# Kernel tuning notes

Hardware: AMD Instinct MI355X
Metric: run time of the kernel (lower is better)

The kernel has to match this reference:

```python
import jax, jax.numpy as jnp
import numpy as np

B, N, C = 128, 36, 1024
K_NB = 16            # neighbors per node (top-k, includes loop)
KERNEL = 8           # number of Gaussian kernels
OUT = 1024           # out_dim; per-kernel out = OUT // KERNEL
PI = np.float32(np.pi)


def setup_inputs() -> dict:
    key = jax.random.key(0)
    ks = jax.random.split(key, 9)
    node_feats = jax.random.normal(ks[0], (B, N, C), dtype=jnp.float32)
    node_centre = jax.random.uniform(ks[1], (B, N, 2), dtype=jnp.float32)
    neighbor_idx = jax.random.randint(ks[2], (B * N, K_NB), 0, B * N, dtype=jnp.int32)
    graph_weights = jax.random.uniform(ks[3], (B * N * K_NB, 1), dtype=jnp.float32)
    # Gaussian kernel params (per reset_parameters)
    mean_rho = jax.random.uniform(ks[4], (1, KERNEL), dtype=jnp.float32)
    mean_theta = jax.random.uniform(ks[5], (1, KERNEL), minval=-PI, maxval=PI, dtype=jnp.float32)
    precision_rho = jax.random.uniform(ks[6], (1, KERNEL), minval=0.5, maxval=1.0, dtype=jnp.float32)
    precision_theta = jax.random.uniform(ks[7], (1, KERNEL), minval=0.5, maxval=1.0, dtype=jnp.float32)
    # per-kernel Linear(node_dim, out_dim//kernel, bias=False), stacked: [K, d_out_k, C]
    conv_w = jax.random.normal(ks[8], (KERNEL, OUT // KERNEL, C), dtype=jnp.float32) * (1.0 / np.sqrt(C))
    return {
        "node_feats": node_feats,
        "node_centre": node_centre,
        "neighbor_idx": neighbor_idx,
        "graph_weights": graph_weights,
        "mean_rho": mean_rho,
        "mean_theta": mean_theta,
        "precision_rho": precision_rho,
        "precision_theta": precision_theta,
        "conv_w": conv_w,
    }


def _forward(node_feats, node_centre, graph_weights,
             mean_rho, mean_theta, precision_rho, precision_theta,
             conv_w, neighbor_idx):
    b, n, c = node_feats.shape
    bn = b * n
    # pseudo polar coordinates per edge: centre_i - centre_j
    centre = node_centre.reshape(bn, 2)                       # [BN, 2]
    diff = centre[:, None, :] - centre[neighbor_idx]          # [BN, K_nb, 2]
    coord_x = diff[..., 0].reshape(-1)                        # [E]
    coord_y = diff[..., 1].reshape(-1)
    rho = jnp.sqrt(coord_x ** 2 + coord_y ** 2)
    theta = jnp.arctan2(coord_x, coord_y)
    # Gaussian mixture membership weights over KERNEL kernels
    w_rho = jnp.exp(-0.5 * (rho[:, None] - mean_rho) ** 2 / (1e-14 + precision_rho ** 2))
    first_angle = jnp.abs(theta[:, None] - mean_theta)
    second_angle = jnp.abs(2.0 * PI - first_angle)
    w_theta = jnp.exp(-0.5 * jnp.minimum(first_angle, second_angle) ** 2 / (1e-14 + precision_theta ** 2))
    weights = w_rho * w_theta                                  # [E, KERNEL]
    weights = jnp.where(jnp.isnan(weights), 0.0, weights)
    weights = weights / jnp.sum(weights, axis=1, keepdims=True)
    # combine with graph edge weights
    edge_w = graph_weights * weights                           # [E, KERNEL]
    edge_w = edge_w.reshape(bn, K_NB, KERNEL).transpose(0, 2, 1)  # [BN, K, K_nb]
    # gather neighbor features and weighted aggregate (bmm)
    nbr = node_feats.reshape(bn, c)[neighbor_idx]              # [BN, K_nb, C]
    agg = jnp.einsum('ekn,enc->ekc', edge_w, nbr)              # [BN, KERNEL, C]
    agg = agg.reshape(b, n, KERNEL, c)
    # per-kernel linear then concat over kernel dim
    out = jnp.einsum('bnkc,kdc->bnkd', agg, conv_w)            # [B, N, KERNEL, OUT//KERNEL]
    out = out.reshape(b, n, -1)                                # [B, N, OUT]
    return jax.nn.relu(out)


def reference(node_feats, node_centre, neighbor_idx, graph_weights,
              mean_rho, mean_theta, precision_rho, precision_theta, conv_w):
    return _forward(node_feats, node_centre, graph_weights,
                    mean_rho, mean_theta, precision_rho, precision_theta,
                    conv_w, neighbor_idx)
```

## Files before the change

### kernel.cpp

```cpp
#include <hip/hip_runtime.h>
#include <hip/hip_bf16.h>
#include <stdint.h>

#define B_DIM   128
#define N_DIM   36
#define C_DIM   1024
#define KNB     16
#define NKER    8
#define OUTD    1024
#define BN_NODES (B_DIM * N_DIM)
#define E_EDGES  (BN_NODES * KNB)
#define PI_F 3.14159265358979323846f

#define TM 128
#define TN 128
#define BK 128
#define CLP 136

typedef __attribute__((ext_vector_type(8))) short bf16x8;
typedef __attribute__((ext_vector_type(4))) float floatx4;

struct alignas(8) U16x4 { unsigned short x, y, z, w; };

__device__ __forceinline__ unsigned short f2bf(float f) {
  union { float f; uint32_t u; } v; v.f = f;
  uint32_t u = v.u;
  return (unsigned short)((u + 0x7fffu + ((u >> 16) & 1u)) >> 16);
}
__device__ __forceinline__ float bf2f(unsigned short h) {
  union { uint32_t u; float f; } v; v.u = ((uint32_t)h) << 16;
  return v.f;
}

__device__ __forceinline__ void gload16(const void* g, void* l) {
  __builtin_amdgcn_global_load_lds((__attribute__((address_space(1))) void*)(g),
                                   (__attribute__((address_space(3))) void*)(l),
                                   16, 0, 0);
}

__global__ __launch_bounds__(256)
void cast_kernel(const float* __restrict__ feats,
                 const float* __restrict__ cw,
                 unsigned short* __restrict__ fb,
                 unsigned short* __restrict__ wb)
{
  const int NF4 = (BN_NODES * C_DIM) / 4;
  const int NW4 = (C_DIM * OUTD) / 4;
  int tid = blockIdx.x * 256 + threadIdx.x;
  if (tid < NF4) {
    float4 v = ((const float4*)feats)[tid];
    U16x4 o = { f2bf(v.x), f2bf(v.y), f2bf(v.z), f2bf(v.w) };
    ((U16x4*)fb)[tid] = o;
  } else {
    int t = tid - NF4;
    if (t < NW4) {
      float4 v = ((const float4*)cw)[t];
      U16x4 o = { f2bf(v.x), f2bf(v.y), f2bf(v.z), f2bf(v.w) };
      ((U16x4*)wb)[t] = o;
    }
  }
}

__global__ __launch_bounds__(256)
void gemm_bt(const unsigned short* __restrict__ A,
             const unsigned short* __restrict__ Bt,
             unsigned short* __restrict__ D)
{
  __shared__ unsigned short smem[TM * BK + TN * BK];
  unsigned short* Al = smem;
  unsigned short* Bl = smem + TM * BK;

  const int tid  = threadIdx.x;
  const int lane = tid & 63;
  const int wave = tid >> 6;
  const int wr   = wave >> 1;
  const int wc   = wave & 1;
  const int row0 = blockIdx.x * TM;
  const int col0 = blockIdx.y * TN;

  const int q  = lane >> 4;
  const int lr = lane & 15;

  floatx4 acc[4][4] = {};

  int offA[8], offB[8];
#pragma unroll
  for (int i = 0; i < 8; ++i) {
    int c   = tid + 256 * i;
    int row = c >> 4, qc = c & 15;
    int sw  = qc ^ (row & 15);
    offA[i] = (row0 + row) * C_DIM + sw * 8;
    offB[i] = (col0 + row) * C_DIM + sw * 8;
  }

  for (int k0 = 0; k0 < C_DIM; k0 += BK) {
#pragma unroll
    for (int i = 0; i < 8; ++i) {
      gload16(A  + offA[i] + k0, &Al[(tid + 256 * i) * 8]);
      gload16(Bt + offB[i] + k0, &Bl[(tid + 256 * i) * 8]);
    }
    __syncthreads();

#pragma unroll
    for (int kc = 0; kc < 4; ++kc) {
      const int sc = ((kc * 4 + q) ^ lr) * 8;
      bf16x8 af[4], bfr[4];
#pragma unroll
      for (int i = 0; i < 4; ++i) {
        af[i]  = *(const bf16x8*)&Al[(wr * 64 + i * 16 + lr) * BK + sc];
        bfr[i] = *(const bf16x8*)&Bl[(wc * 64 + i * 16 + lr) * BK + sc];
      }
#pragma unroll
      for (int i = 0; i < 4; ++i)
#pragma unroll
        for (int j = 0; j < 4; ++j)
          acc[i][j] = __builtin_amdgcn_mfma_f32_16x16x32_bf16(
              af[i], bfr[j], acc[i][j], 0, 0, 0);
    }
    __syncthreads();
  }

  unsigned short* Cl = smem;
#pragma unroll
  for (int i = 0; i < 4; ++i)
#pragma unroll
    for (int j = 0; j < 4; ++j)
#pragma unroll
      for (int r = 0; r < 4; ++r)
        Cl[(wr * 64 + i * 16 + q * 4 + r) * CLP + wc * 64 + j * 16 + lr] =
            f2bf(acc[i][j][r]);
  __syncthreads();
#pragma unroll
  for (int i = 0; i < 8; ++i) {
    int c = tid + 256 * i;
    int row = c >> 4, qc = c & 15;
    *(uint4*)&D[(size_t)(row0 + row) * OUTD + col0 + qc * 8] =
        *(const uint4*)&Cl[row * CLP + qc * 8];
  }
}

__global__ __launch_bounds__(256)
void agg_fused(const unsigned short* __restrict__ proj,
               const float* __restrict__ centre,
               const int*   __restrict__ nbr,
               const float* __restrict__ gw,
               const float* __restrict__ mrho,
               const float* __restrict__ mth,
               const float* __restrict__ prho,
               const float* __restrict__ pth,
               float* __restrict__ out)
{
  __shared__ int   idx[KNB];
  __shared__ float nx[KNB], ny[KNB];
  __shared__ float cc[2];
  __shared__ float wk[KNB][NKER];
  __shared__ float scl[KNB];
  __shared__ float ew[NKER][KNB];

  const int n = blockIdx.x;
  const int t = threadIdx.x;

  if (t < KNB) {
    int m = nbr[n * KNB + t];
    idx[t] = m;
    nx[t] = centre[2 * m];
    ny[t] = centre[2 * m + 1];
  } else if (t == KNB) {
    cc[0] = centre[2 * n];
    cc[1] = centre[2 * n + 1];
  }
  __syncthreads();

  if (t < 128) {
    int j = t >> 3, k = t & 7;
    float cx = cc[0] - nx[j];
    float cy = cc[1] - ny[j];
    float rho   = sqrtf(cx * cx + cy * cy);
    float theta = atan2f(cx, cy);
    float dr = rho - mrho[k];
    float pr = prho[k];
    float w_r = expf(-0.5f * dr * dr / (1e-14f + pr * pr));
    float fa = fabsf(theta - mth[k]);
    float sa = fabsf(2.0f * PI_F - fa);
    float mm = fminf(fa, sa);
    float pt = pth[k];
    float w_t = expf(-0.5f * mm * mm / (1e-14f + pt * pt));
    float ww = w_r * w_t;
    wk[j][k] = (ww != ww) ? 0.f : ww;
  }
  __syncthreads();

  if (t < KNB) {
    float s = 0.f;
#pragma unroll
    for (int k = 0; k < NKER; ++k) s += wk[t][k];
    scl[t] = gw[n * KNB + t] / s;
  }
  __syncthreads();

  if (t < 128) {
    int j = t >> 3, k = t & 7;
    ew[k][j] = wk[j][k] * scl[j];
  }
  __syncthreads();

  const int k = t >> 5;
  float a0 = 0.f, a1 = 0.f, a2 = 0.f, a3 = 0.f;
#pragma unroll
  for (int j = 0; j < KNB; ++j) {
    float wv = ew[k][j];
    U16x4 v = *(const U16x4*)&proj[(size_t)idx[j] * OUTD + t * 4];
    a0 += wv * bf2f(v.x);
    a1 += wv * bf2f(v.y);
    a2 += wv * bf2f(v.z);
    a3 += wv * bf2f(v.w);
  }
  float4 r;
  r.x = fmaxf(a0, 0.f); r.y = fmaxf(a1, 0.f);
  r.z = fmaxf(a2, 0.f); r.w = fmaxf(a3, 0.f);
  ((float4*)out)[(size_t)n * (OUTD / 4) + t] = r;
}

extern "C" void kernel_launch(void* const* d_in, const int* in_sizes, int n_in,
                              void* d_out, int out_size, void* d_ws, size_t ws_size,
                              hipStream_t stream)
{
  const float* feats  = (const float*)d_in[0];
  const float* centre = (const float*)d_in[1];
  const int*   nbr    = (const int*)  d_in[2];
  const float* gw     = (const float*)d_in[3];
  const float* mrho   = (const float*)d_in[4];
  const float* mth    = (const float*)d_in[5];
  const float* prho   = (const float*)d_in[6];
  const float* pth    = (const float*)d_in[7];
  const float* cw     = (const float*)d_in[8];
  float* out = (float*)d_out;

  char* ws = (char*)d_ws;
  unsigned short* fb   = (unsigned short*)(ws);
  unsigned short* wb   = (unsigned short*)(ws + 9437184);
  unsigned short* proj = (unsigned short*)(ws + 11534336);

  cast_kernel<<<dim3(((BN_NODES * C_DIM) / 4 + (C_DIM * OUTD) / 4) / 256),
                dim3(256), 0, stream>>>(feats, cw, fb, wb);
  gemm_bt<<<dim3(BN_NODES / TM, OUTD / TN), dim3(256), 0, stream>>>(fb, wb, proj);
  agg_fused<<<dim3(BN_NODES), dim3(256), 0, stream>>>(
      proj, centre, nbr, gw, mrho, mth, prho, pth, out);
}
```

Before: 126.9 us.

## Double-buffer GEMM shared-memory tiles with BK=64 to overlap loads and MFMA

Splits the K loop into 64-wide tiles and ping-pongs two shared-memory buffers for A and B. The async load of the next tile is issued right after the barrier, so it runs during the MFMA work on the current tile. The XOR swizzle is adjusted to the 8-chunk row width. This halves the number of barriers per tile but depends on the compiler's wait placement for the async LDS loads.

```diff
diff --git a/kernel.cpp b/kernel.cpp
--- a/kernel.cpp
+++ b/kernel.cpp
@@ -14,7 +14,8 @@
 
 #define TM 128
 #define TN 128
-#define BK 128
+#define BK 64
+#define KIT (C_DIM / BK)
 #define CLP 136
 
 typedef __attribute__((ext_vector_type(8))) short bf16x8;
@@ -66,9 +67,7 @@
              const unsigned short* __restrict__ Bt,
              unsigned short* __restrict__ D)
 {
-  __shared__ unsigned short smem[TM * BK + TN * BK];
-  unsigned short* Al = smem;
-  unsigned short* Bl = smem + TM * BK;
+  __shared__ unsigned short smem[4 * TM * BK];
 
   const int tid  = threadIdx.x;
   const int lane = tid & 63;
@@ -83,32 +82,42 @@
 
   floatx4 acc[4][4] = {};
 
-  int offA[8], offB[8];
-#pragma unroll
-  for (int i = 0; i < 8; ++i) {
+  int offA[4], offB[4];
+#pragma unroll
+  for (int i = 0; i < 4; ++i) {
     int c   = tid + 256 * i;
-    int row = c >> 4, qc = c & 15;
-    int sw  = qc ^ (row & 15);
+    int row = c >> 3, qc = c & 7;
+    int sw  = qc ^ (row & 7);
     offA[i] = (row0 + row) * C_DIM + sw * 8;
     offB[i] = (col0 + row) * C_DIM + sw * 8;
   }
 
-  for (int k0 = 0; k0 < C_DIM; k0 += BK) {
-#pragma unroll
-    for (int i = 0; i < 8; ++i) {
-      gload16(A  + offA[i] + k0, &Al[(tid + 256 * i) * 8]);
-      gload16(Bt + offB[i] + k0, &Bl[(tid + 256 * i) * 8]);
-    }
+#define DMA(T, P) do {                                                       \
+    _Pragma("unroll") for (int i = 0; i < 4; ++i) {                          \
+      gload16(A  + offA[i] + (T) * BK,                                       \
+              &smem[(P) * TM * BK + (tid + 256 * i) * 8]);                   \
+      gload16(Bt + offB[i] + (T) * BK,                                       \
+              &smem[(2 + (P)) * TM * BK + (tid + 256 * i) * 8]);             \
+    }                                                                        \
+  } while (0)
+
+  DMA(0, 0);
+
+  for (int t = 0; t < KIT; ++t) {
+    const int p = t & 1;
     __syncthreads();
-
-#pragma unroll
-    for (int kc = 0; kc < 4; ++kc) {
-      const int sc = ((kc * 4 + q) ^ lr) * 8;
+    if (t + 1 < KIT) DMA(t + 1, 1 - p);
+
+    const int aBase = p * TM * BK;
+    const int bBase = (2 + p) * TM * BK;
+#pragma unroll
+    for (int kc = 0; kc < 2; ++kc) {
+      const int sc = ((kc * 4 + q) ^ (lr & 7)) * 8;
       bf16x8 af[4], bfr[4];
 #pragma unroll
       for (int i = 0; i < 4; ++i) {
-        af[i]  = *(const bf16x8*)&Al[(wr * 64 + i * 16 + lr) * BK + sc];
-        bfr[i] = *(const bf16x8*)&Bl[(wc * 64 + i * 16 + lr) * BK + sc];
+        af[i]  = *(const bf16x8*)&smem[aBase + (wr * 64 + i * 16 + lr) * BK + sc];
+        bfr[i] = *(const bf16x8*)&smem[bBase + (wc * 64 + i * 16 + lr) * BK + sc];
       }
 #pragma unroll
       for (int i = 0; i < 4; ++i)
@@ -117,17 +126,17 @@
           acc[i][j] = __builtin_amdgcn_mfma_f32_16x16x32_bf16(
               af[i], bfr[j], acc[i][j], 0, 0, 0);
     }
-    __syncthreads();
-  }
-
-  unsigned short* Cl = smem;
+  }
+#undef DMA
+
+  __syncthreads();
 #pragma unroll
   for (int i = 0; i < 4; ++i)
 #pragma unroll
     for (int j = 0; j < 4; ++j)
 #pragma unroll
       for (int r = 0; r < 4; ++r)
-        Cl[(wr * 64 + i * 16 + q * 4 + r) * CLP + wc * 64 + j * 16 + lr] =
+        smem[(wr * 64 + i * 16 + q * 4 + r) * CLP + wc * 64 + j * 16 + lr] =
             f2bf(acc[i][j][r]);
   __syncthreads();
 #pragma unroll
@@ -135,7 +144,7 @@
     int c = tid + 256 * i;
     int row = c >> 4, qc = c & 15;
     *(uint4*)&D[(size_t)(row0 + row) * OUTD + col0 + qc * 8] =
-        *(const uint4*)&Cl[row * CLP + qc * 8];
+        *(const uint4*)&smem[row * CLP + qc * 8];
   }
 }
 
```

New measurement: 126.0 us. About the same (-0.7%).
